# Performance work log

Hardware: AMD Instinct MI355X
Metric: run time of the kernel (lower is better)

Reference implementation:

```python
import jax, jax.numpy as jnp
import numpy as np

B, S, D = 64, 2048, 512


def setup_inputs() -> dict:
    key = jax.random.key(0)
    k1, k2, k3, k4 = jax.random.split(key, 4)
    decoder_output = jax.random.normal(k1, (B, 1, D), dtype=jnp.float32)
    encoder_output = jax.random.normal(k2, (B, S, D), dtype=jnp.float32)
    # W_a_tanh: Dense(D) applied to concat([dec, enc]) of width 2D
    scale_w = 1.0 / np.sqrt(2 * D)
    W_t = jax.random.normal(k3, (2 * D, D), dtype=jnp.float32) * scale_w
    b_t = jnp.zeros((D,), dtype=jnp.float32)
    # v_a: Dense(1)
    v_a = jax.random.normal(k4, (D, 1), dtype=jnp.float32) * (1.0 / np.sqrt(D))
    b_v = jnp.zeros((1,), dtype=jnp.float32)
    return {
        "decoder_output": decoder_output,
        "encoder_output": encoder_output,
        "W_t": W_t,
        "b_t": b_t,
        "v_a": v_a,
        "b_v": b_v,
    }


def reference(decoder_output, encoder_output, W_t, b_t, v_a, b_v):
    # concat-variant Luong attention
    dec = jnp.broadcast_to(decoder_output, encoder_output.shape)       # [B,S,D]
    concated = jnp.concatenate((dec, encoder_output), axis=-1)          # [B,S,2D]
    hidden = jnp.tanh(jnp.einsum('bse,ed->bsd', concated, W_t) + b_t)   # [B,S,D]
    score = (jnp.einsum('bsd,do->bso', hidden, v_a) + b_v)              # [B,S,1]
    score = jnp.transpose(score, (0, 2, 1))                             # [B,1,S]
    alignment_vector = jax.nn.softmax(score, axis=2)                    # [B,1,S]
    context_vector = jnp.matmul(alignment_vector, encoder_output)       # [B,1,D]
    return (context_vector, alignment_vector)
```

## Files before the change

### kernel.cpp

```cpp
#include <hip/hip_runtime.h>
#include <hip/hip_bf16.h>

#define BB 64
#define SS 2048
#define DD 512
#define MM (BB * SS)

typedef __attribute__((ext_vector_type(8))) short bf16x8;
typedef __attribute__((ext_vector_type(4))) float f32x4;

__device__ __forceinline__ unsigned f2bf(float f) {
    unsigned u = __float_as_uint(f);
    u += 0x7FFFu + ((u >> 16) & 1u);
    return u >> 16;
}

__device__ __forceinline__ float fast_tanh(float x) {
    float ax = fabsf(x);
    float e = __expf(-2.0f * ax);
    float t = (1.0f - e) * __builtin_amdgcn_rcpf(1.0f + e);
    return x < 0.0f ? -t : t;
}

__global__ void prep_w(const float* __restrict__ W, short* __restrict__ Bt) {
    int idx = blockIdx.x * 256 + threadIdx.x;
    int n = idx >> 9;
    int k = idx & 511;
    Bt[idx] = (short)f2bf(W[(size_t)(512 + k) * DD + n]);
}

__global__ void prep_p(const float* __restrict__ dec, const float* __restrict__ W,
                       const float* __restrict__ bt, float* __restrict__ p) {
    int b = blockIdx.x;
    int d = blockIdx.y * 256 + threadIdx.x;
    float acc = bt[d];
    const float* dv = dec + (size_t)b * DD;
    #pragma unroll 8
    for (int e = 0; e < DD; ++e)
        acc += dv[e] * W[(size_t)e * DD + d];
    p[(size_t)b * DD + d] = acc;
}

__launch_bounds__(256)
__global__ void score_gemm(const float* __restrict__ enc,
                           const short* __restrict__ Bt,
                           const float* __restrict__ p,
                           const float* __restrict__ va,
                           const float* __restrict__ bv,
                           float* __restrict__ score) {
    __shared__ short Alds[64 * 32];
    __shared__ short Blds[512 * 32];
    __shared__ float sp[4][64];

    const int tid  = threadIdx.x;
    const int wave = tid >> 6;
    const int lane = tid & 63;
    const int m0   = blockIdx.x * 64;

    f32x4 acc[4][8];
    #pragma unroll
    for (int i = 0; i < 4; ++i)
        #pragma unroll
        for (int j = 0; j < 8; ++j)
            acc[i][j] = (f32x4){0.f, 0.f, 0.f, 0.f};

    const int arow = tid >> 2;
    const int acol = (tid & 3) * 8;
    const float* aptr = enc + (size_t)(m0 + arow) * DD + acol;

    const int brow0 = wave * 128 + (lane >> 2);
    const int bcoff = (lane & 3) * 8;
    const short* bptr = Bt + (size_t)brow0 * DD + bcoff;

    const int lm = lane & 15;
    const int lq = lane >> 4;

    for (int kt = 0; kt < 16; ++kt) {
        const int k0 = kt * 32;
        __syncthreads();
        f32x4 a0 = *(const f32x4*)(aptr + k0);
        f32x4 a1 = *(const f32x4*)(aptr + k0 + 4);
        int4 pk;
        pk.x = f2bf(a0.x) | (f2bf(a0.y) << 16);
        pk.y = f2bf(a0.z) | (f2bf(a0.w) << 16);
        pk.z = f2bf(a1.x) | (f2bf(a1.y) << 16);
        pk.w = f2bf(a1.z) | (f2bf(a1.w) << 16);
        *(int4*)(&Alds[arow * 32 + acol]) = pk;
        #pragma unroll
        for (int i = 0; i < 8; ++i) {
            __builtin_amdgcn_global_load_lds(
                (const __attribute__((address_space(1))) void*)(bptr + (size_t)i * 16 * DD + k0),
                (__attribute__((address_space(3))) void*)(&Blds[(wave * 128 + i * 16) * 32]),
                16, 0, 0);
        }
        __syncthreads();
        bf16x8 af[4];
        #pragma unroll
        for (int mf = 0; mf < 4; ++mf)
            af[mf] = *(const bf16x8*)(&Alds[(mf * 16 + lm) * 32 + lq * 8]);
        #pragma unroll
        for (int nf = 0; nf < 8; ++nf) {
            bf16x8 bfr = *(const bf16x8*)(&Blds[(wave * 128 + nf * 16 + lm) * 32 + lq * 8]);
            #pragma unroll
            for (int mf = 0; mf < 4; ++mf)
                acc[mf][nf] = __builtin_amdgcn_mfma_f32_16x16x32_bf16(af[mf], bfr, acc[mf][nf], 0, 0, 0);
        }
    }

    const int b = m0 >> 11;
    float rowsum[4][4];
    #pragma unroll
    for (int mf = 0; mf < 4; ++mf)
        #pragma unroll
        for (int r = 0; r < 4; ++r) rowsum[mf][r] = 0.f;

    #pragma unroll
    for (int nf = 0; nf < 8; ++nf) {
        int n = wave * 128 + nf * 16 + lm;
        float pv = p[(size_t)b * DD + n];
        float vv = va[n];
        #pragma unroll
        for (int mf = 0; mf < 4; ++mf)
            #pragma unroll
            for (int r = 0; r < 4; ++r)
                rowsum[mf][r] += fast_tanh(pv + acc[mf][nf][r]) * vv;
    }
    #pragma unroll
    for (int mf = 0; mf < 4; ++mf)
        #pragma unroll
        for (int r = 0; r < 4; ++r) {
            float s = rowsum[mf][r];
            s += __shfl_xor(s, 1);
            s += __shfl_xor(s, 2);
            s += __shfl_xor(s, 4);
            s += __shfl_xor(s, 8);
            rowsum[mf][r] = s;
        }
    if (lm == 0) {
        #pragma unroll
        for (int mf = 0; mf < 4; ++mf)
            #pragma unroll
            for (int r = 0; r < 4; ++r)
                sp[wave][mf * 16 + lq * 4 + r] = rowsum[mf][r];
    }
    __syncthreads();
    if (tid < 64) {
        float sc = sp[0][tid] + sp[1][tid] + sp[2][tid] + sp[3][tid] + bv[0];
        score[(size_t)m0 + tid] = sc;
    }
}

__global__ void softmax_k(const float* __restrict__ score, float* __restrict__ align) {
    __shared__ float red[256];
    int b = blockIdx.x, tid = threadIdx.x;
    const float* s = score + (size_t)b * SS;
    float vals[8];
    float mx = -1e30f;
    #pragma unroll
    for (int i = 0; i < 8; ++i) {
        vals[i] = s[i * 256 + tid];
        mx = fmaxf(mx, vals[i]);
    }
    red[tid] = mx; __syncthreads();
    for (int off = 128; off > 0; off >>= 1) {
        if (tid < off) red[tid] = fmaxf(red[tid], red[tid + off]);
        __syncthreads();
    }
    mx = red[0]; __syncthreads();
    float sum = 0.f;
    #pragma unroll
    for (int i = 0; i < 8; ++i) {
        vals[i] = __expf(vals[i] - mx);
        sum += vals[i];
    }
    red[tid] = sum; __syncthreads();
    for (int off = 128; off > 0; off >>= 1) {
        if (tid < off) red[tid] += red[tid + off];
        __syncthreads();
    }
    float inv = 1.0f / red[0];
    #pragma unroll
    for (int i = 0; i < 8; ++i)
        align[(size_t)b * SS + i * 256 + tid] = vals[i] * inv;
}

__global__ void context_k(const float* __restrict__ enc, const float* __restrict__ align,
                          float* __restrict__ ctx) {
    int bx = blockIdx.x;
    int b = bx >> 4, chunk = bx & 15;
    int tid = threadIdx.x;
    const float2* e2 = (const float2*)(enc + ((size_t)b * SS + chunk * 128) * DD);
    const float* a = align + (size_t)b * SS + chunk * 128;
    float2 acc = {0.f, 0.f};
    #pragma unroll 4
    for (int s = 0; s < 128; ++s) {
        float av = a[s];
        float2 e = e2[(size_t)s * 256 + tid];
        acc.x += av * e.x;
        acc.y += av * e.y;
    }
    atomicAdd(&ctx[(size_t)b * DD + tid * 2], acc.x);
    atomicAdd(&ctx[(size_t)b * DD + tid * 2 + 1], acc.y);
}

extern "C" void kernel_launch(void* const* d_in, const int* in_sizes, int n_in,
                              void* d_out, int out_size, void* d_ws, size_t ws_size,
                              hipStream_t stream) {
    const float* dec = (const float*)d_in[0];
    const float* enc = (const float*)d_in[1];
    const float* W   = (const float*)d_in[2];
    const float* bt  = (const float*)d_in[3];
    const float* va  = (const float*)d_in[4];
    const float* bv  = (const float*)d_in[5];

    float* out   = (float*)d_out;
    float* ctx   = out;
    float* align = out + BB * DD;

    char*  ws    = (char*)d_ws;
    short* Bt    = (short*)ws;
    float* p     = (float*)(ws + 512 * 512 * 2);
    float* score = (float*)(ws + 512 * 512 * 2 + BB * DD * 4);

    hipMemsetAsync(ctx, 0, BB * DD * sizeof(float), stream);
    prep_w<<<1024, 256, 0, stream>>>(W, Bt);
    prep_p<<<dim3(BB, 2), 256, 0, stream>>>(dec, W, bt, p);
    score_gemm<<<MM / 64, 256, 0, stream>>>(enc, Bt, p, va, bv, score);
    softmax_k<<<BB, 256, 0, stream>>>(score, align);
    context_k<<<BB * 16, 256, 0, stream>>>(enc, align, ctx);
}
```

Before: 604.5 us.

## Double-buffer score GEMM, retile to 128x256 blocks, transpose W via LDS

```diff
diff --git a/kernel.cpp b/kernel.cpp
--- a/kernel.cpp
+++ b/kernel.cpp
@@ -23,10 +23,23 @@
 }
 
 __global__ void prep_w(const float* __restrict__ W, short* __restrict__ Bt) {
-    int idx = blockIdx.x * 256 + threadIdx.x;
-    int n = idx >> 9;
-    int k = idx & 511;
-    Bt[idx] = (short)f2bf(W[(size_t)(512 + k) * DD + n]);
+    __shared__ float tile[64][65];
+    int kt = blockIdx.x >> 3;
+    int nt = blockIdx.x & 7;
+    int t = threadIdx.x;
+    int c = t & 63;
+    int rbase = (t >> 6) * 16;
+    #pragma unroll
+    for (int i = 0; i < 16; ++i) {
+        int r = rbase + i;
+        tile[r][c] = W[(size_t)(512 + kt * 64 + r) * DD + nt * 64 + c];
+    }
+    __syncthreads();
+    #pragma unroll
+    for (int i = 0; i < 16; ++i) {
+        int r = rbase + i;
+        Bt[(size_t)(nt * 64 + r) * DD + kt * 64 + c] = (short)f2bf(tile[c][r]);
+    }
 }
 
 __global__ void prep_p(const float* __restrict__ dec, const float* __restrict__ W,
@@ -41,21 +54,25 @@
     p[(size_t)b * DD + d] = acc;
 }
 
-__launch_bounds__(256)
-__global__ void score_gemm(const float* __restrict__ enc,
-                           const short* __restrict__ Bt,
-                           const float* __restrict__ p,
-                           const float* __restrict__ va,
-                           const float* __restrict__ bv,
-                           float* __restrict__ score) {
-    __shared__ short Alds[64 * 32];
-    __shared__ short Blds[512 * 32];
+__global__ __launch_bounds__(256)
+void score_gemm(const float* __restrict__ enc,
+                const short* __restrict__ Bt,
+                const float* __restrict__ p,
+                const float* __restrict__ va,
+                float* __restrict__ score) {
+    __shared__ short Alds[2][128 * 32];
+    __shared__ short Blds[2][256 * 32];
     __shared__ float sp[4][64];
 
     const int tid  = threadIdx.x;
     const int wave = tid >> 6;
     const int lane = tid & 63;
-    const int m0   = blockIdx.x * 64;
+    const int mblk = blockIdx.x >> 1;
+    const int n0   = (blockIdx.x & 1) * 256;
+    const int m0   = mblk * 128;
+
+    const int wm = wave >> 1, wn = wave & 1;
+    const int lm = lane & 15, lq = lane >> 4;
 
     f32x4 acc[4][8];
     #pragma unroll
@@ -66,45 +83,78 @@
 
     const int arow = tid >> 2;
     const int acol = (tid & 3) * 8;
-    const float* aptr = enc + (size_t)(m0 + arow) * DD + acol;
-
-    const int brow0 = wave * 128 + (lane >> 2);
-    const int bcoff = (lane & 3) * 8;
-    const short* bptr = Bt + (size_t)brow0 * DD + bcoff;
-
-    const int lm = lane & 15;
-    const int lq = lane >> 4;
+    const float* aptr0 = enc + (size_t)(m0 + arow) * DD + acol;
+    const float* aptr1 = aptr0 + (size_t)64 * DD;
+
+    const short* bptr = Bt + (size_t)(n0 + wave * 64 + (lane >> 2)) * DD + (lane & 3) * 8;
+
+    #pragma unroll
+    for (int i = 0; i < 4; ++i)
+        __builtin_amdgcn_global_load_lds(
+            (const __attribute__((address_space(1))) void*)(bptr + (size_t)i * 16 * DD),
+            (__attribute__((address_space(3))) void*)(&Blds[0][(wave * 64 + i * 16) * 32]),
+            16, 0, 0);
+    {
+        f32x4 x0 = *(const f32x4*)(aptr0);
+        f32x4 x1 = *(const f32x4*)(aptr0 + 4);
+        f32x4 y0 = *(const f32x4*)(aptr1);
+        f32x4 y1 = *(const f32x4*)(aptr1 + 4);
+        int4 px, py;
+        px.x = f2bf(x0.x) | (f2bf(x0.y) << 16);
+        px.y = f2bf(x0.z) | (f2bf(x0.w) << 16);
+        px.z = f2bf(x1.x) | (f2bf(x1.y) << 16);
+        px.w = f2bf(x1.z) | (f2bf(x1.w) << 16);
+        py.x = f2bf(y0.x) | (f2bf(y0.y) << 16);
+        py.y = f2bf(y0.z) | (f2bf(y0.w) << 16);
+        py.z = f2bf(y1.x) | (f2bf(y1.y) << 16);
+        py.w = f2bf(y1.z) | (f2bf(y1.w) << 16);
+        *(int4*)(&Alds[0][arow * 32 + acol]) = px;
+        *(int4*)(&Alds[0][(arow + 64) * 32 + acol]) = py;
+    }
+    __syncthreads();
 
     for (int kt = 0; kt < 16; ++kt) {
-        const int k0 = kt * 32;
-        __syncthreads();
-        f32x4 a0 = *(const f32x4*)(aptr + k0);
-        f32x4 a1 = *(const f32x4*)(aptr + k0 + 4);
-        int4 pk;
-        pk.x = f2bf(a0.x) | (f2bf(a0.y) << 16);
-        pk.y = f2bf(a0.z) | (f2bf(a0.w) << 16);
-        pk.z = f2bf(a1.x) | (f2bf(a1.y) << 16);
-        pk.w = f2bf(a1.z) | (f2bf(a1.w) << 16);
-        *(int4*)(&Alds[arow * 32 + acol]) = pk;
-        #pragma unroll
-        for (int i = 0; i < 8; ++i) {
-            __builtin_amdgcn_global_load_lds(
-                (const __attribute__((address_space(1))) void*)(bptr + (size_t)i * 16 * DD + k0),
-                (__attribute__((address_space(3))) void*)(&Blds[(wave * 128 + i * 16) * 32]),
-                16, 0, 0);
-        }
-        __syncthreads();
+        const int c = kt & 1;
+        const bool pf = kt < 15;
+        f32x4 x0, x1, y0, y1;
+        if (pf) {
+            const int kn = (kt + 1) * 32;
+            #pragma unroll
+            for (int i = 0; i < 4; ++i)
+                __builtin_amdgcn_global_load_lds(
+                    (const __attribute__((address_space(1))) void*)(bptr + (size_t)i * 16 * DD + kn),
+                    (__attribute__((address_space(3))) void*)(&Blds[1 - c][(wave * 64 + i * 16) * 32]),
+                    16, 0, 0);
+            x0 = *(const f32x4*)(aptr0 + kn);
+            x1 = *(const f32x4*)(aptr0 + kn + 4);
+            y0 = *(const f32x4*)(aptr1 + kn);
+            y1 = *(const f32x4*)(aptr1 + kn + 4);
+        }
         bf16x8 af[4];
         #pragma unroll
         for (int mf = 0; mf < 4; ++mf)
-            af[mf] = *(const bf16x8*)(&Alds[(mf * 16 + lm) * 32 + lq * 8]);
+            af[mf] = *(const bf16x8*)(&Alds[c][(wm * 64 + mf * 16 + lm) * 32 + lq * 8]);
         #pragma unroll
         for (int nf = 0; nf < 8; ++nf) {
-            bf16x8 bfr = *(const bf16x8*)(&Blds[(wave * 128 + nf * 16 + lm) * 32 + lq * 8]);
+            bf16x8 bfr = *(const bf16x8*)(&Blds[c][(wn * 128 + nf * 16 + lm) * 32 + lq * 8]);
             #pragma unroll
             for (int mf = 0; mf < 4; ++mf)
                 acc[mf][nf] = __builtin_amdgcn_mfma_f32_16x16x32_bf16(af[mf], bfr, acc[mf][nf], 0, 0, 0);
         }
+        if (pf) {
+            int4 px, py;
+            px.x = f2bf(x0.x) | (f2bf(x0.y) << 16);
+            px.y = f2bf(x0.z) | (f2bf(x0.w) << 16);
+            px.z = f2bf(x1.x) | (f2bf(x1.y) << 16);
+            px.w = f2bf(x1.z) | (f2bf(x1.w) << 16);
+            py.x = f2bf(y0.x) | (f2bf(y0.y) << 16);
+            py.y = f2bf(y0.z) | (f2bf(y0.w) << 16);
+            py.z = f2bf(y1.x) | (f2bf(y1.y) << 16);
+            py.w = f2bf(y1.z) | (f2bf(y1.w) << 16);
+            *(int4*)(&Alds[1 - c][arow * 32 + acol]) = px;
+            *(int4*)(&Alds[1 - c][(arow + 64) * 32 + acol]) = py;
+        }
+        __syncthreads();
     }
 
     const int b = m0 >> 11;
@@ -116,7 +166,7 @@
 
     #pragma unroll
     for (int nf = 0; nf < 8; ++nf) {
-        int n = wave * 128 + nf * 16 + lm;
+        int n = n0 + wn * 128 + nf * 16 + lm;
         float pv = p[(size_t)b * DD + n];
         float vv = va[n];
         #pragma unroll
@@ -144,9 +194,10 @@
                 sp[wave][mf * 16 + lq * 4 + r] = rowsum[mf][r];
     }
     __syncthreads();
-    if (tid < 64) {
-        float sc = sp[0][tid] + sp[1][tid] + sp[2][tid] + sp[3][tid] + bv[0];
-        score[(size_t)m0 + tid] = sc;
+    if (tid < 128) {
+        int row = tid & 63, half = tid >> 6;
+        float v = sp[half * 2][row] + sp[half * 2 + 1][row];
+        atomicAdd(&score[(size_t)m0 + half * 64 + row], v);
     }
 }
 
@@ -211,7 +262,6 @@
     const float* W   = (const float*)d_in[2];
     const float* bt  = (const float*)d_in[3];
     const float* va  = (const float*)d_in[4];
-    const float* bv  = (const float*)d_in[5];
 
     float* out   = (float*)d_out;
     float* ctx   = out;
@@ -223,9 +273,10 @@
     float* score = (float*)(ws + 512 * 512 * 2 + BB * DD * 4);
 
     hipMemsetAsync(ctx, 0, BB * DD * sizeof(float), stream);
-    prep_w<<<1024, 256, 0, stream>>>(W, Bt);
+    hipMemsetAsync(score, 0, MM * sizeof(float), stream);
+    prep_w<<<64, 256, 0, stream>>>(W, Bt);
     prep_p<<<dim3(BB, 2), 256, 0, stream>>>(dec, W, bt, p);
-    score_gemm<<<MM / 64, 256, 0, stream>>>(enc, Bt, p, va, bv, score);
+    score_gemm<<<MM / 64, 256, 0, stream>>>(enc, Bt, p, va, score);
     softmax_k<<<BB, 256, 0, stream>>>(score, align);
     context_k<<<BB * 16, 256, 0, stream>>>(enc, align, ctx);
 }
```

Measured after the change: 593.8 us. About the same (-1.8%).
